# Performance work log

Hardware: AMD Instinct MI355X
Metric: run time of the kernel (lower is better)

## Reference

```python
import jax, jax.numpy as jnp
import numpy as np

N = 512          # input_dim (nodes, fully connected)
T = 16           # time_dim
F = 4            # feature_dim
D = T * F        # node_attr_dim = 64
B = 16           # batch
NEG_SLOPE = 0.2  # GATv2Conv default


def setup_inputs() -> dict:
    key = jax.random.key(0)
    ks = jax.random.split(key, 10)
    s = 0.05
    return {
        "inputs": jax.random.normal(ks[0], (B, N * D), dtype=jnp.float32),
        "Wl": jax.random.normal(ks[1], (D, D), dtype=jnp.float32) * s,  # lin_l weight
        "bl": jax.random.normal(ks[2], (D,), dtype=jnp.float32) * s,
        "Wr": jax.random.normal(ks[3], (D, D), dtype=jnp.float32) * s,  # lin_r weight
        "br": jax.random.normal(ks[4], (D,), dtype=jnp.float32) * s,
        "att": jax.random.normal(ks[5], (D,), dtype=jnp.float32) * s,   # attention vector a
        "bias": jax.random.normal(ks[6], (D,), dtype=jnp.float32) * s,  # GATv2 output bias
        "Wf": jax.random.normal(ks[7], (1, D), dtype=jnp.float32) * s,  # fusion Linear
        "bf": jax.random.normal(ks[8], (1,), dtype=jnp.float32) * s,
    }


def reference(inputs, Wl, bl, Wr, br, att, bias, Wf, bf):
    # GATv2Conv (heads=1) over a fully-connected graph -> dense attention per sample.
    def per_sample(x_flat):
        x = x_flat.reshape(N, D)              # [N, D] node features
        xl = x @ Wl.T + bl                    # source-side transform (lin_l)
        xr = x @ Wr.T + br                    # target-side transform (lin_r)
        # edge (j -> i): e_ij = a . leaky_relu(xl[j] + xr[i])
        s = jax.nn.leaky_relu(xr[:, None, :] + xl[None, :, :], NEG_SLOPE)  # [i, j, d]
        e = jnp.einsum('ijd,d->ij', s, att)   # [N, N] scores
        alpha = jax.nn.softmax(e, axis=-1)    # softmax over sources j per target i
        out = alpha @ xl + bias               # [N, D] aggregated messages
        fused = out @ Wf.T + bf               # [N, 1] fusion linear
        return fused[:, 0]                    # [N]

    return jax.vmap(per_sample)(inputs)       # [B, N]
```

## Files before the change

kernel.cpp:

```cpp
#include <hip/hip_runtime.h>
#include <hip/hip_fp16.h>

#define BB 16
#define NN 512
#define DD 64
#define ROWS (BB * NN)
#define ITILE 8
#define RB 16

static __device__ __forceinline__ __half2 h2bits(unsigned int u) {
    union { unsigned int i; __half2 h; } c; c.i = u; return c.h;
}
static __device__ __forceinline__ unsigned int bits2(__half2 h) {
    union { __half2 h; unsigned int i; } c; c.h = h; return c.i;
}

__global__ __launch_bounds__(256, 4) void k1_transform(
    const float* __restrict__ x,
    const float* __restrict__ Wl, const float* __restrict__ bl,
    const float* __restrict__ Wr, const float* __restrict__ br,
    const float* __restrict__ att, const float* __restrict__ bias,
    const float* __restrict__ Wf, const float* __restrict__ bf,
    unsigned int* __restrict__ uh, unsigned int* __restrict__ vh,
    float* __restrict__ axl, float* __restrict__ pxl,
    unsigned int* __restrict__ sgnh, float* __restrict__ cterm)
{
    __shared__ float wt[64][132];
    __shared__ float xs[RB][66];
    __shared__ float red[RB][16][2];

    const int tid = threadIdx.x;
    const int r0 = blockIdx.x * RB;

    #pragma unroll
    for (int t = 0; t < 8; ++t) {
        const int idx = t * 256 + tid;
        const int c   = idx & 127;
        const int k4  = (idx >> 7) * 4;
        const float* src = (c < 64) ? (Wl + c * DD + k4) : (Wr + (c - 64) * DD + k4);
        const float4 v = *reinterpret_cast<const float4*>(src);
        wt[k4 + 0][c] = v.x;
        wt[k4 + 1][c] = v.y;
        wt[k4 + 2][c] = v.z;
        wt[k4 + 3][c] = v.w;
    }
    {
        const int row = tid >> 4, q = tid & 15;
        const float4 v = *reinterpret_cast<const float4*>(&x[(size_t)(r0 + row) * DD + q * 4]);
        xs[row][q * 4 + 0] = v.x;
        xs[row][q * 4 + 1] = v.y;
        xs[row][q * 4 + 2] = v.z;
        xs[row][q * 4 + 3] = v.w;
    }
    __syncthreads();

    const int g  = tid & 31;
    const int rp = tid >> 5;
    const int c0 = g * 4;
    const int ra = rp * 2, rb = ra + 1;
    const bool isL = (c0 < 64);
    const int d0 = c0 & 63;

    const float4 bv = *reinterpret_cast<const float4*>((isL ? bl : br) + d0);
    float acc[2][4];
    #pragma unroll
    for (int r = 0; r < 2; ++r) {
        acc[r][0] = bv.x; acc[r][1] = bv.y; acc[r][2] = bv.z; acc[r][3] = bv.w;
    }

    #pragma unroll 4
    for (int k = 0; k < 64; ++k) {
        const float4 w4 = *reinterpret_cast<const float4*>(&wt[k][c0]);
        const float xa = xs[ra][k];
        const float xb = xs[rb][k];
        acc[0][0] = fmaf(xa, w4.x, acc[0][0]);
        acc[0][1] = fmaf(xa, w4.y, acc[0][1]);
        acc[0][2] = fmaf(xa, w4.z, acc[0][2]);
        acc[0][3] = fmaf(xa, w4.w, acc[0][3]);
        acc[1][0] = fmaf(xb, w4.x, acc[1][0]);
        acc[1][1] = fmaf(xb, w4.y, acc[1][1]);
        acc[1][2] = fmaf(xb, w4.z, acc[1][2]);
        acc[1][3] = fmaf(xb, w4.w, acc[1][3]);
    }

    const float4 av = *reinterpret_cast<const float4*>(&att[d0]);

    if (isL) {
        const float4 wfv = *reinterpret_cast<const float4*>(&Wf[d0]);
        #pragma unroll
        for (int r = 0; r < 2; ++r) {
            const float pa = av.x * acc[r][0] + av.y * acc[r][1] + av.z * acc[r][2] + av.w * acc[r][3];
            const float pp = wfv.x * acc[r][0] + wfv.y * acc[r][1] + wfv.z * acc[r][2] + wfv.w * acc[r][3];
            red[ra + r][g][0] = pa;
            red[ra + r][g][1] = pp;
        }
    }

    unsigned int* const dst = isL ? vh : uh;
    #pragma unroll
    for (int r = 0; r < 2; ++r) {
        uint2 pk;
        pk.x = bits2(__floats2half2_rn(0.4f * av.x * acc[r][0], 0.4f * av.y * acc[r][1]));
        pk.y = bits2(__floats2half2_rn(0.4f * av.z * acc[r][2], 0.4f * av.w * acc[r][3]));
        *reinterpret_cast<uint2*>(&dst[(size_t)(r0 + ra + r) * 32 + (d0 >> 1)]) = pk;
    }
    __syncthreads();

    if (tid < 32) {
        const int row = tid >> 1, which = tid & 1;
        float s = 0.f;
        #pragma unroll
        for (int gg = 0; gg < 16; ++gg) s += red[row][gg][which];
        if (which) pxl[r0 + row] = s;
        else       axl[r0 + row] = s;
    }

    if (blockIdx.x == 0) {
        if (tid < 32) {
            const float s0 = (att[2 * tid]     >= 0.f) ? 1.f : -1.f;
            const float s1 = (att[2 * tid + 1] >= 0.f) ? 1.f : -1.f;
            sgnh[tid] = bits2(__floats2half2_rn(s0, s1));
        }
        if (tid == 0) {
            float ct = bf[0];
            #pragma unroll 8
            for (int d = 0; d < DD; ++d) ct = fmaf(bias[d], Wf[d], ct);
            *cterm = ct;
        }
    }
}

__global__ __launch_bounds__(512, 8) void k2_attn(
    const unsigned int* __restrict__ uh, const unsigned int* __restrict__ vh,
    const float* __restrict__ axl, const float* __restrict__ pxl,
    const unsigned int* __restrict__ sgnh, const float* __restrict__ cterm,
    float* __restrict__ out)
{
    __shared__ unsigned int us[ITILE][32];
    __shared__ float e[ITILE][NN];

    const int tid = threadIdx.x;
    const int b  = blockIdx.x >> 6;
    const int i0 = (blockIdx.x & 63) * ITILE;

    if (tid < 64) {
        const int ir = tid >> 3, c4 = (tid & 7) * 4;
        *reinterpret_cast<uint4*>(&us[ir][c4]) =
            *reinterpret_cast<const uint4*>(&uh[((size_t)(b * NN + i0 + ir)) * 32 + c4]);
    }

    const int j = tid;
    const size_t rowj = (size_t)b * NN + j;
    const float axlj = 0.6f * axl[rowj];
    __syncthreads();

    __half2 acc[ITILE];
    #pragma unroll
    for (int i = 0; i < ITILE; ++i) acc[i] = __float2half2_rn(0.f);

    const uint4* const vbase = reinterpret_cast<const uint4*>(&vh[rowj * 32]);
    const uint4* const sbase = reinterpret_cast<const uint4*>(sgnh);

    #pragma unroll 1
    for (int c = 0; c < 4; ++c) {
        const uint4 v0 = vbase[c * 2 + 0];
        const uint4 v1 = vbase[c * 2 + 1];
        const uint4 s0 = sbase[c * 2 + 0];
        const uint4 s1 = sbase[c * 2 + 1];
        #pragma unroll
        for (int i = 0; i < ITILE; ++i) {
            const uint4 u0 = *reinterpret_cast<const uint4*>(&us[i][c * 8 + 0]);
            const uint4 u1 = *reinterpret_cast<const uint4*>(&us[i][c * 8 + 4]);
            __half2 a = acc[i];
            a = __hfma2(h2bits(s0.x), __habs2(__hadd2(h2bits(u0.x), h2bits(v0.x))), a);
            a = __hfma2(h2bits(s0.y), __habs2(__hadd2(h2bits(u0.y), h2bits(v0.y))), a);
            a = __hfma2(h2bits(s0.z), __habs2(__hadd2(h2bits(u0.z), h2bits(v0.z))), a);
            a = __hfma2(h2bits(s0.w), __habs2(__hadd2(h2bits(u0.w), h2bits(v0.w))), a);
            a = __hfma2(h2bits(s1.x), __habs2(__hadd2(h2bits(u1.x), h2bits(v1.x))), a);
            a = __hfma2(h2bits(s1.y), __habs2(__hadd2(h2bits(u1.y), h2bits(v1.y))), a);
            a = __hfma2(h2bits(s1.z), __habs2(__hadd2(h2bits(u1.z), h2bits(v1.z))), a);
            a = __hfma2(h2bits(s1.w), __habs2(__hadd2(h2bits(u1.w), h2bits(v1.w))), a);
            acc[i] = a;
        }
    }

    #pragma unroll
    for (int i = 0; i < ITILE; ++i)
        e[i][j] = axlj + __low2float(acc[i]) + __high2float(acc[i]);
    __syncthreads();

    const int wv = tid >> 6;
    const int lane = tid & 63;

    float pv[8], vals[8];
    #pragma unroll
    for (int k = 0; k < 8; ++k) pv[k] = pxl[(size_t)b * NN + lane + 64 * k];
    #pragma unroll
    for (int k = 0; k < 8; ++k) vals[k] = e[wv][lane + 64 * k];

    float m = vals[0];
    #pragma unroll
    for (int k = 1; k < 8; ++k) m = fmaxf(m, vals[k]);
    #pragma unroll
    for (int mask = 32; mask >= 1; mask >>= 1)
        m = fmaxf(m, __shfl_xor(m, mask));

    float s = 0.f, sp = 0.f;
    #pragma unroll
    for (int k = 0; k < 8; ++k) {
        const float t = __expf(vals[k] - m);
        s += t;
        sp = fmaf(t, pv[k], sp);
    }
    #pragma unroll
    for (int mask = 32; mask >= 1; mask >>= 1) {
        s  += __shfl_xor(s, mask);
        sp += __shfl_xor(sp, mask);
    }
    if (lane == 0)
        out[(size_t)b * NN + i0 + wv] = sp / s + *cterm;
}

extern "C" void kernel_launch(void* const* d_in, const int* in_sizes, int n_in,
                              void* d_out, int out_size, void* d_ws, size_t ws_size,
                              hipStream_t stream) {
    const float* x    = (const float*)d_in[0];
    const float* Wl   = (const float*)d_in[1];
    const float* bl   = (const float*)d_in[2];
    const float* Wr   = (const float*)d_in[3];
    const float* br   = (const float*)d_in[4];
    const float* att  = (const float*)d_in[5];
    const float* bias = (const float*)d_in[6];
    const float* Wf   = (const float*)d_in[7];
    const float* bf   = (const float*)d_in[8];
    float* out = (float*)d_out;

    unsigned char* ws = (unsigned char*)d_ws;
    unsigned int* uh   = (unsigned int*)ws;
    unsigned int* vh   = uh + (size_t)ROWS * 32;
    float*        axl  = (float*)(vh + (size_t)ROWS * 32);
    float*        pxl  = axl + ROWS;
    unsigned int* sgnh = (unsigned int*)(pxl + ROWS);
    float*        ctp  = (float*)(sgnh + 32);

    k1_transform<<<ROWS / RB, 256, 0, stream>>>(x, Wl, bl, Wr, br, att, bias, Wf, bf,
                                                uh, vh, axl, pxl, sgnh, ctp);
    k2_attn<<<BB * (NN / ITILE), 512, 0, stream>>>(uh, vh, axl, pxl, sgnh, ctp, out);
}
```

Measured before the change: 28.73 us.

## Enlarge transform row tile and restructure attention score loop over register-held keys

The transform kernel now processes 32 rows per block, with the input tile stored transposed so each thread reads a float4 of four rows per k step and computes a 4x4 register tile, which doubles weight reuse. Launch bounds drop to 2 blocks per SM. The attention kernel keeps each source node's 64 half-precision values in registers, drops the shared-memory staging of target rows and one barrier, and reads target rows directly from global/L2 with two independent accumulators per target to shorten dependency chains. The costs are higher register pressure and redundant global loads of target rows that are the same for every thread.

```diff
diff --git a/kernel.cpp b/kernel.cpp
--- a/kernel.cpp
+++ b/kernel.cpp
@@ -6,7 +6,7 @@
 #define DD 64
 #define ROWS (BB * NN)
 #define ITILE 8
-#define RB 16
+#define RB 32
 
 static __device__ __forceinline__ __half2 h2bits(unsigned int u) {
     union { unsigned int i; __half2 h; } c; c.i = u; return c.h;
@@ -14,8 +14,12 @@
 static __device__ __forceinline__ unsigned int bits2(__half2 h) {
     union { __half2 h; unsigned int i; } c; c.h = h; return c.i;
 }
-
-__global__ __launch_bounds__(256, 4) void k1_transform(
+static __device__ __forceinline__ __half2 absterm(unsigned int s, unsigned int u,
+                                                  unsigned int v, __half2 a) {
+    return __hfma2(h2bits(s), __habs2(__hadd2(h2bits(u), h2bits(v))), a);
+}
+
+__global__ __launch_bounds__(256, 2) void k1_transform(
     const float* __restrict__ x,
     const float* __restrict__ Wl, const float* __restrict__ bl,
     const float* __restrict__ Wr, const float* __restrict__ br,
@@ -26,7 +30,7 @@
     unsigned int* __restrict__ sgnh, float* __restrict__ cterm)
 {
     __shared__ float wt[64][132];
-    __shared__ float xs[RB][66];
+    __shared__ float xst[64][36];
     __shared__ float red[RB][16][2];
 
     const int tid = threadIdx.x;
@@ -36,7 +40,7 @@
     for (int t = 0; t < 8; ++t) {
         const int idx = t * 256 + tid;
         const int c   = idx & 127;
-        const int k4  = (idx >> 7) * 4;
+        const int k4  = (idx >> 7) << 2;
         const float* src = (c < 64) ? (Wl + c * DD + k4) : (Wr + (c - 64) * DD + k4);
         const float4 v = *reinterpret_cast<const float4*>(src);
         wt[k4 + 0][c] = v.x;
@@ -44,43 +48,53 @@
         wt[k4 + 2][c] = v.z;
         wt[k4 + 3][c] = v.w;
     }
-    {
-        const int row = tid >> 4, q = tid & 15;
-        const float4 v = *reinterpret_cast<const float4*>(&x[(size_t)(r0 + row) * DD + q * 4]);
-        xs[row][q * 4 + 0] = v.x;
-        xs[row][q * 4 + 1] = v.y;
-        xs[row][q * 4 + 2] = v.z;
-        xs[row][q * 4 + 3] = v.w;
+    #pragma unroll
+    for (int p = 0; p < 2; ++p) {
+        const int idx = p * 256 + tid;
+        const int row = idx >> 4;
+        const int k4  = (idx & 15) << 2;
+        const float4 v = *reinterpret_cast<const float4*>(&x[(size_t)(r0 + row) * DD + k4]);
+        xst[k4 + 0][row] = v.x;
+        xst[k4 + 1][row] = v.y;
+        xst[k4 + 2][row] = v.z;
+        xst[k4 + 3][row] = v.w;
     }
     __syncthreads();
 
     const int g  = tid & 31;
-    const int rp = tid >> 5;
+    const int rq = tid >> 5;
     const int c0 = g * 4;
-    const int ra = rp * 2, rb = ra + 1;
+    const int ra = rq * 4;
     const bool isL = (c0 < 64);
     const int d0 = c0 & 63;
 
     const float4 bv = *reinterpret_cast<const float4*>((isL ? bl : br) + d0);
-    float acc[2][4];
-    #pragma unroll
-    for (int r = 0; r < 2; ++r) {
+    float acc[4][4];
+    #pragma unroll
+    for (int r = 0; r < 4; ++r) {
         acc[r][0] = bv.x; acc[r][1] = bv.y; acc[r][2] = bv.z; acc[r][3] = bv.w;
     }
 
     #pragma unroll 4
     for (int k = 0; k < 64; ++k) {
         const float4 w4 = *reinterpret_cast<const float4*>(&wt[k][c0]);
-        const float xa = xs[ra][k];
-        const float xb = xs[rb][k];
-        acc[0][0] = fmaf(xa, w4.x, acc[0][0]);
-        acc[0][1] = fmaf(xa, w4.y, acc[0][1]);
-        acc[0][2] = fmaf(xa, w4.z, acc[0][2]);
-        acc[0][3] = fmaf(xa, w4.w, acc[0][3]);
-        acc[1][0] = fmaf(xb, w4.x, acc[1][0]);
-        acc[1][1] = fmaf(xb, w4.y, acc[1][1]);
-        acc[1][2] = fmaf(xb, w4.z, acc[1][2]);
-        acc[1][3] = fmaf(xb, w4.w, acc[1][3]);
+        const float4 x4 = *reinterpret_cast<const float4*>(&xst[k][ra]);
+        acc[0][0] = fmaf(x4.x, w4.x, acc[0][0]);
+        acc[0][1] = fmaf(x4.x, w4.y, acc[0][1]);
+        acc[0][2] = fmaf(x4.x, w4.z, acc[0][2]);
+        acc[0][3] = fmaf(x4.x, w4.w, acc[0][3]);
+        acc[1][0] = fmaf(x4.y, w4.x, acc[1][0]);
+        acc[1][1] = fmaf(x4.y, w4.y, acc[1][1]);
+        acc[1][2] = fmaf(x4.y, w4.z, acc[1][2]);
+        acc[1][3] = fmaf(x4.y, w4.w, acc[1][3]);
+        acc[2][0] = fmaf(x4.z, w4.x, acc[2][0]);
+        acc[2][1] = fmaf(x4.z, w4.y, acc[2][1]);
+        acc[2][2] = fmaf(x4.z, w4.z, acc[2][2]);
+        acc[2][3] = fmaf(x4.z, w4.w, acc[2][3]);
+        acc[3][0] = fmaf(x4.w, w4.x, acc[3][0]);
+        acc[3][1] = fmaf(x4.w, w4.y, acc[3][1]);
+        acc[3][2] = fmaf(x4.w, w4.z, acc[3][2]);
+        acc[3][3] = fmaf(x4.w, w4.w, acc[3][3]);
     }
 
     const float4 av = *reinterpret_cast<const float4*>(&att[d0]);
@@ -88,17 +102,15 @@
     if (isL) {
         const float4 wfv = *reinterpret_cast<const float4*>(&Wf[d0]);
         #pragma unroll
-        for (int r = 0; r < 2; ++r) {
-            const float pa = av.x * acc[r][0] + av.y * acc[r][1] + av.z * acc[r][2] + av.w * acc[r][3];
-            const float pp = wfv.x * acc[r][0] + wfv.y * acc[r][1] + wfv.z * acc[r][2] + wfv.w * acc[r][3];
-            red[ra + r][g][0] = pa;
-            red[ra + r][g][1] = pp;
+        for (int r = 0; r < 4; ++r) {
+            red[ra + r][g][0] = av.x * acc[r][0] + av.y * acc[r][1] + av.z * acc[r][2] + av.w * acc[r][3];
+            red[ra + r][g][1] = wfv.x * acc[r][0] + wfv.y * acc[r][1] + wfv.z * acc[r][2] + wfv.w * acc[r][3];
         }
     }
 
     unsigned int* const dst = isL ? vh : uh;
     #pragma unroll
-    for (int r = 0; r < 2; ++r) {
+    for (int r = 0; r < 4; ++r) {
         uint2 pk;
         pk.x = bits2(__floats2half2_rn(0.4f * av.x * acc[r][0], 0.4f * av.y * acc[r][1]));
         pk.y = bits2(__floats2half2_rn(0.4f * av.z * acc[r][2], 0.4f * av.w * acc[r][3]));
@@ -106,7 +118,7 @@
     }
     __syncthreads();
 
-    if (tid < 32) {
+    if (tid < 64) {
         const int row = tid >> 1, which = tid & 1;
         float s = 0.f;
         #pragma unroll
@@ -136,57 +148,40 @@
     const unsigned int* __restrict__ sgnh, const float* __restrict__ cterm,
     float* __restrict__ out)
 {
-    __shared__ unsigned int us[ITILE][32];
     __shared__ float e[ITILE][NN];
 
     const int tid = threadIdx.x;
     const int b  = blockIdx.x >> 6;
     const int i0 = (blockIdx.x & 63) * ITILE;
-
-    if (tid < 64) {
-        const int ir = tid >> 3, c4 = (tid & 7) * 4;
-        *reinterpret_cast<uint4*>(&us[ir][c4]) =
-            *reinterpret_cast<const uint4*>(&uh[((size_t)(b * NN + i0 + ir)) * 32 + c4]);
-    }
-
     const int j = tid;
     const size_t rowj = (size_t)b * NN + j;
+
+    uint4 vv[8];
+    const uint4* const vb = reinterpret_cast<const uint4*>(&vh[rowj * 32]);
+    #pragma unroll
+    for (int q = 0; q < 8; ++q) vv[q] = vb[q];
+
+    const uint4* const sb = reinterpret_cast<const uint4*>(sgnh);
     const float axlj = 0.6f * axl[rowj];
-    __syncthreads();
-
-    __half2 acc[ITILE];
-    #pragma unroll
-    for (int i = 0; i < ITILE; ++i) acc[i] = __float2half2_rn(0.f);
-
-    const uint4* const vbase = reinterpret_cast<const uint4*>(&vh[rowj * 32]);
-    const uint4* const sbase = reinterpret_cast<const uint4*>(sgnh);
-
-    #pragma unroll 1
-    for (int c = 0; c < 4; ++c) {
-        const uint4 v0 = vbase[c * 2 + 0];
-        const uint4 v1 = vbase[c * 2 + 1];
-        const uint4 s0 = sbase[c * 2 + 0];
-        const uint4 s1 = sbase[c * 2 + 1];
+
+    #pragma unroll 2
+    for (int i = 0; i < ITILE; ++i) {
+        const uint4* const ub =
+            reinterpret_cast<const uint4*>(&uh[(size_t)(b * NN + i0 + i) * 32]);
+        __half2 a0 = __float2half2_rn(0.f), a1 = a0;
         #pragma unroll
-        for (int i = 0; i < ITILE; ++i) {
-            const uint4 u0 = *reinterpret_cast<const uint4*>(&us[i][c * 8 + 0]);
-            const uint4 u1 = *reinterpret_cast<const uint4*>(&us[i][c * 8 + 4]);
-            __half2 a = acc[i];
-            a = __hfma2(h2bits(s0.x), __habs2(__hadd2(h2bits(u0.x), h2bits(v0.x))), a);
-            a = __hfma2(h2bits(s0.y), __habs2(__hadd2(h2bits(u0.y), h2bits(v0.y))), a);
-            a = __hfma2(h2bits(s0.z), __habs2(__hadd2(h2bits(u0.z), h2bits(v0.z))), a);
-            a = __hfma2(h2bits(s0.w), __habs2(__hadd2(h2bits(u0.w), h2bits(v0.w))), a);
-            a = __hfma2(h2bits(s1.x), __habs2(__hadd2(h2bits(u1.x), h2bits(v1.x))), a);
-            a = __hfma2(h2bits(s1.y), __habs2(__hadd2(h2bits(u1.y), h2bits(v1.y))), a);
-            a = __hfma2(h2bits(s1.z), __habs2(__hadd2(h2bits(u1.z), h2bits(v1.z))), a);
-            a = __hfma2(h2bits(s1.w), __habs2(__hadd2(h2bits(u1.w), h2bits(v1.w))), a);
-            acc[i] = a;
-        }
-    }
-
-    #pragma unroll
-    for (int i = 0; i < ITILE; ++i)
-        e[i][j] = axlj + __low2float(acc[i]) + __high2float(acc[i]);
+        for (int q = 0; q < 8; ++q) {
+            const uint4 uu = ub[q];
+            const uint4 sq = sb[q];
+            const uint4 vq = vv[q];
+            a0 = absterm(sq.x, uu.x, vq.x, a0);
+            a1 = absterm(sq.y, uu.y, vq.y, a1);
+            a0 = absterm(sq.z, uu.z, vq.z, a0);
+            a1 = absterm(sq.w, uu.w, vq.w, a1);
+        }
+        const __half2 h = __hadd2(a0, a1);
+        e[i][j] = axlj + __low2float(h) + __high2float(h);
+    }
     __syncthreads();
 
     const int wv = tid >> 6;
```

Result: slower. 30.71 us (+6.9%).
